# Kernel optimization log

Hardware: AMD Instinct MI355X
Metric: run time of the kernel (lower is better)

Reference implementation:

```python
import jax, jax.numpy as jnp
import numpy as np

N_NODES = 100_000
N_EDGES = 1_600_000
N_GRAPHS = 512
IN_C, HID_C, OUT_C = 17, 64, 32


def setup_inputs() -> dict:
    key = jax.random.key(0)
    ks = jax.random.split(key, 12)
    x = jax.random.normal(ks[0], (N_NODES, IN_C), dtype=jnp.float32)
    edge_index = jax.random.randint(ks[1], (2, N_EDGES), 0, N_NODES, dtype=jnp.int64)
    batch = jnp.sort(jax.random.randint(ks[2], (N_NODES,), 0, N_GRAPHS, dtype=jnp.int64))
    def lin(k, fan_in, fan_out):
        s = 1.0 / np.sqrt(fan_in)
        kw, kb = jax.random.split(k)
        W = jax.random.uniform(kw, (fan_in, fan_out), minval=-s, maxval=s, dtype=jnp.float32)
        b = jax.random.uniform(kb, (fan_out,), minval=-s, maxval=s, dtype=jnp.float32)
        return W, b
    W1, b1 = lin(ks[3], IN_C, HID_C)      # GCNConv 1
    W2, b2 = lin(ks[4], HID_C, OUT_C)     # GCNConv 2
    Wf1, bf1 = lin(ks[5], OUT_C, OUT_C)   # fc1
    Wf2, bf2 = lin(ks[6], OUT_C, OUT_C)   # fc2
    return {"x": x, "edge_index": edge_index, "batch": batch,
            "W1": W1, "b1": b1, "W2": W2, "b2": b2,
            "Wf1": Wf1, "bf1": bf1, "Wf2": Wf2, "bf2": bf2}


def _gcn_conv(x, src, dst, norm, W, b, n_nodes):
    # PyG GCNConv: h = x @ W; out_i = sum_{j->i} norm_ij * h_j; out += bias
    h = x @ W                                   # [N, d_out]
    msg = h[src] * norm[:, None]                # gather + scale [E+N, d_out]
    out = jax.ops.segment_sum(msg, dst, num_segments=n_nodes)
    return out + b


def reference(x, edge_index, batch, W1, b1, W2, b2, Wf1, bf1, Wf2, bf2):
    n = x.shape[0]
    loops = jnp.arange(n, dtype=edge_index.dtype)
    src = jnp.concatenate([edge_index[0], loops])  # add self loops
    dst = jnp.concatenate([edge_index[1], loops])
    # symmetric normalization: deg^-1/2[src] * deg^-1/2[dst]
    deg = jax.ops.segment_sum(jnp.ones_like(dst, dtype=x.dtype), dst, num_segments=n)
    dinv = jnp.where(deg > 0, 1.0 / jnp.sqrt(deg), 0.0)
    norm = dinv[src] * dinv[dst]

    h = jax.nn.relu(_gcn_conv(x, src, dst, norm, W1, b1, n))
    h = _gcn_conv(h, src, dst, norm, W2, b2, n)

    # global mean pool over graphs
    cnt = jax.ops.segment_sum(jnp.ones((n,), dtype=h.dtype), batch, num_segments=N_GRAPHS)
    pooled = jax.ops.segment_sum(h, batch, num_segments=N_GRAPHS) / jnp.clip(cnt, 1.0)[:, None]

    out = jax.nn.relu(pooled @ Wf1 + bf1)
    out = out @ Wf2 + bf2
    return out  # [N_GRAPHS, OUT_C]
```

## Files before the change

### kernel.cpp

```cpp
#include <hip/hip_runtime.h>

#define IN_C 17
#define HID  64
#define OUTC 32

#define CH   8192
#define TA   512
#define NBP  512
#define BCAP 5632
#define SCAP 1024
#define BS_BLKS 8

typedef __attribute__((ext_vector_type(2))) float f2;
__device__ __forceinline__ f2 mkf2(float x, float y) { f2 r; r.x = x; r.y = y; return r; }

__device__ __forceinline__ unsigned short f2bf(float f) {
    unsigned u = __float_as_uint(f);
    u += 0x7fffu + ((u >> 16) & 1u);
    return (unsigned short)(u >> 16);
}
__device__ __forceinline__ float bflo(unsigned u) { return __uint_as_float(u << 16); }
__device__ __forceinline__ float bfhi(unsigned u) { return __uint_as_float(u & 0xffff0000u); }

__global__ __launch_bounds__(TA) void k_binA(const int* __restrict__ src,
        const int* __restrict__ dst, int E,
        int* __restrict__ outbuf, int* __restrict__ cntmat, int* __restrict__ offmat) {
    __shared__ int cnt[NBP];
    __shared__ int off[NBP];
    __shared__ int stage[CH];
    int t = threadIdx.x;
    long base = (long)blockIdx.x * CH;
    int nE = (int)(E - base); if (nE > CH) nE = CH;
    cnt[t] = 0;
    __syncthreads();
    int bk[16], pk[16], rk[16];
#pragma unroll
    for (int j = 0; j < 16; ++j) {
        int idx = t + j * TA;
        if (idx < nE) {
            long e = base + idx;
            int d = __builtin_nontemporal_load(&dst[e]);
            int s = __builtin_nontemporal_load(&src[e]);
            int b = d >> 8;
            bk[j] = b;
            pk[j] = s | ((d & 255) << 17);
            rk[j] = atomicAdd(&cnt[b], 1);
        } else bk[j] = -1;
    }
    __syncthreads();
    int c = cnt[t];
    off[t] = c;
    __syncthreads();
    int inc = c;
    for (int s = 1; s < NBP; s <<= 1) {
        int add = (t >= s) ? off[t - s] : 0;
        __syncthreads();
        inc += add; off[t] = inc;
        __syncthreads();
    }
    int excl = inc - c;
    __syncthreads();
    off[t] = excl;
    __syncthreads();
#pragma unroll
    for (int j = 0; j < 16; ++j)
        if (bk[j] >= 0) stage[off[bk[j]] + rk[j]] = pk[j];
    __syncthreads();
    for (int i = t; i < nE; i += TA) outbuf[base + i] = stage[i];
    cntmat[blockIdx.x * NBP + t] = c;
    offmat[blockIdx.x * NBP + t] = excl;
}

__global__ __launch_bounds__(NBP) void k_bsum1(const int* __restrict__ cntmat,
        int nblkA, int* __restrict__ part) {
    int t = threadIdx.x, b = blockIdx.x;
    int per = (nblkA + BS_BLKS - 1) / BS_BLKS;
    int i0 = b * per, i1 = min(i0 + per, nblkA);
    int s = 0;
    for (int i = i0; i < i1; ++i) s += cntmat[i * NBP + t];
    part[b * NBP + t] = s;
}

__global__ __launch_bounds__(NBP) void k_bsum2(const int* __restrict__ part,
        int* __restrict__ bbase) {
    __shared__ int sh[NBP];
    int t = threadIdx.x;
    int s = 0;
#pragma unroll
    for (int i = 0; i < BS_BLKS; ++i) s += part[i * NBP + t];
    sh[t] = s;
    __syncthreads();
    int inc = s;
    for (int st = 1; st < NBP; st <<= 1) {
        int add = (t >= st) ? sh[t - st] : 0;
        __syncthreads();
        inc += add; sh[t] = inc;
        __syncthreads();
    }
    bbase[t] = inc - s;
}

__global__ __launch_bounds__(TA) void k_binB(const int* __restrict__ outbuf,
        const int* __restrict__ cntmat, const int* __restrict__ offmat,
        const int* __restrict__ bbase, int nblkA, int N,
        int* __restrict__ csr, int2* __restrict__ meta,
        const float* __restrict__ x, unsigned* __restrict__ xs16h,
        unsigned short* __restrict__ xs17h) {
    __shared__ int segc[256], sego[256], segs[256];
    __shared__ int ndeg[256], noff[256];
    __shared__ int stage[BCAP];
    int t = threadIdx.x, b = blockIdx.x;
    if (t < 256) {
        int cc = 0, ss = 0;
        if (t < nblkA) { cc = cntmat[t * NBP + b]; ss = offmat[t * NBP + b]; }
        segc[t] = cc; segs[t] = ss; sego[t] = cc;
        ndeg[t] = 0;
    }
    __syncthreads();
    {
        int c = (t < 256) ? sego[t] : 0;
        int inc = c;
        for (int s = 1; s < 256; s <<= 1) {
            int add = (t < 256 && t >= s) ? sego[t - s] : 0;
            __syncthreads();
            if (t < 256) { inc += add; sego[t] = inc; }
            __syncthreads();
        }
        if (t < 256) sego[t] = inc - c;
    }
    __syncthreads();
    int wave = t >> 6, lane = t & 63;
    for (int i = wave; i < nblkA; i += TA / 64) {
        int c = segc[i], so = sego[i];
        long gs = (long)i * CH + segs[i];
        for (int l = lane; l < c; l += 64) {
            int p = so + l;
            if (p < BCAP) stage[p] = __builtin_nontemporal_load(&outbuf[gs + l]);
        }
    }
    __syncthreads();
    int T = sego[255] + segc[255];
    if (T > BCAP) T = BCAP;
    int mypk[11], myrk[11], ne = 0;
    for (int k = t; k < T; k += TA) {
        int p = stage[k];
        int l = (p >> 17) & 255;
        myrk[ne] = atomicAdd(&ndeg[l], 1);
        mypk[ne] = p;
        ne++;
    }
    __syncthreads();
    {
        int c = (t < 256) ? ndeg[t] : 0;
        if (t < 256) noff[t] = c;
        __syncthreads();
        int inc = c;
        for (int s = 1; s < 256; s <<= 1) {
            int add = (t < 256 && t >= s) ? noff[t - s] : 0;
            __syncthreads();
            if (t < 256) { inc += add; noff[t] = inc; }
            __syncthreads();
        }
        if (t < 256) noff[t] = inc - c;
    }
    __syncthreads();
    int gb = bbase[b];
    int n0 = b << 8;
    if (t < 256 && n0 + t < N) {
        int n = n0 + t;
        meta[n] = make_int2(gb + noff[t], ndeg[t]);
        float dinv = rsqrtf((float)(ndeg[t] + 1));
        const float* xr = x + (size_t)n * IN_C;
        unsigned* xo = xs16h + (size_t)n * 8;
#pragma unroll
        for (int w2 = 0; w2 < 8; ++w2) {
            unsigned lo = f2bf(xr[2 * w2] * dinv);
            unsigned hi = f2bf(xr[2 * w2 + 1] * dinv);
            xo[w2] = lo | (hi << 16);
        }
        xs17h[n] = f2bf(xr[16] * dinv);
    }
    for (int j = 0; j < ne; ++j) {
        int p = mypk[j];
        int l = (p >> 17) & 255;
        csr[gb + noff[l] + myrk[j]] = p & 0x1FFFF;
    }
}

__global__ __launch_bounds__(256) void k_gather1(
        const uint4* __restrict__ xs16v, const unsigned short* __restrict__ xs17h,
        const int* __restrict__ csr, const int2* __restrict__ meta,
        const float* __restrict__ W1, const float* __restrict__ b1,
        const float* __restrict__ W2, unsigned* __restrict__ hs2, int N) {
    __shared__ __align__(16) float aggx[16][20];
    __shared__ float dinv_sh[16];
    __shared__ __align__(16) float h1sh[16][68];
    __shared__ __align__(16) float w2c0[16][68];
    __shared__ __align__(16) float w2c1[16][68];
    __shared__ int csr_sh[SCAP];

    int tid = threadIdx.x;
    int n0 = blockIdx.x * 16;
    int nlast = min(n0 + 15, N - 1);
    int2 m0 = meta[n0];
    int2 mlv = meta[nlast];
    int s_lo = m0.x;
    int seglen = mlv.x + mlv.y - s_lo;
    int sg = min(seglen, SCAP);
    for (int i = tid; i < sg; i += 256)
        csr_sh[i] = __builtin_nontemporal_load(&csr[s_lo + i]);
    for (int i = tid; i < 16 * 64; i += 256) {
        int tc = i >> 6, k = i & 63;
        w2c0[tc][k] = W2[k * OUTC + 2 * tc];
        w2c1[tc][k] = W2[k * OUTC + 2 * tc + 1];
    }
    int ch = tid & 63;
    float w1r[IN_C];
#pragma unroll
    for (int k = 0; k < IN_C; ++k) w1r[k] = W1[k * HID + ch];
    float b1v = b1[ch];
    __syncthreads();

    int ln = tid >> 4, sl = tid & 15;
    int n = n0 + ln;
    f2 acc[8];
#pragma unroll
    for (int j = 0; j < 8; ++j) acc[j] = mkf2(0.f, 0.f);
    float a17 = 0.f;
    if (n < N) {
        int2 m = meta[n];
        int start = m.x, cnt = m.y, end = start + cnt;
        auto body = [&](int s) {
            uint4 v0 = xs16v[(size_t)s * 2];
            uint4 v1 = xs16v[(size_t)s * 2 + 1];
            acc[0] += mkf2(bflo(v0.x), bfhi(v0.x));
            acc[1] += mkf2(bflo(v0.y), bfhi(v0.y));
            acc[2] += mkf2(bflo(v0.z), bfhi(v0.z));
            acc[3] += mkf2(bflo(v0.w), bfhi(v0.w));
            acc[4] += mkf2(bflo(v1.x), bfhi(v1.x));
            acc[5] += mkf2(bflo(v1.y), bfhi(v1.y));
            acc[6] += mkf2(bflo(v1.z), bfhi(v1.z));
            acc[7] += mkf2(bflo(v1.w), bfhi(v1.w));
            a17 += bflo((unsigned)xs17h[s]);
        };
        if (seglen <= SCAP) {
            for (int k = start + sl; k < end; k += 16) body(csr_sh[k - s_lo]);
        } else {
            for (int k = start + sl; k < end; k += 16)
                body(__builtin_nontemporal_load(&csr[k]));
        }
        if (sl == 0) {
            body(n);
            dinv_sh[ln] = rsqrtf((float)(cnt + 1));
        }
    }
    float a[16];
#pragma unroll
    for (int j = 0; j < 8; ++j) { a[2 * j] = acc[j].x; a[2 * j + 1] = acc[j].y; }
#pragma unroll
    for (int j = 0; j < 8; ++j) {
        float tt = (sl & 8) ? a[j + 8] : a[j];
        float uu = (sl & 8) ? a[j] : a[j + 8];
        a[j] = tt + __shfl_xor(uu, 8);
    }
#pragma unroll
    for (int j = 0; j < 4; ++j) {
        float tt = (sl & 4) ? a[j + 4] : a[j];
        float uu = (sl & 4) ? a[j] : a[j + 4];
        a[j] = tt + __shfl_xor(uu, 4);
    }
#pragma unroll
    for (int j = 0; j < 2; ++j) {
        float tt = (sl & 2) ? a[j + 2] : a[j];
        float uu = (sl & 2) ? a[j] : a[j + 2];
        a[j] = tt + __shfl_xor(uu, 2);
    }
    {
        float tt = (sl & 1) ? a[1] : a[0];
        float uu = (sl & 1) ? a[0] : a[1];
        a[0] = tt + __shfl_xor(uu, 1);
    }
    a17 += __shfl_xor(a17, 1);
    a17 += __shfl_xor(a17, 2);
    a17 += __shfl_xor(a17, 4);
    a17 += __shfl_xor(a17, 8);
    aggx[ln][sl] = a[0];
    if (sl == 0) aggx[ln][16] = a17;
    __syncthreads();
    int s0 = tid >> 6;
#pragma unroll
    for (int rep = 0; rep < 4; ++rep) {
        int slot = s0 + rep * 4;
        int nn = n0 + slot;
        if (nn < N) {
            const float4* ap = (const float4*)aggx[slot];
            float4 A0 = ap[0], A1 = ap[1], A2 = ap[2], A3 = ap[3];
            float a16 = aggx[slot][16];
            float dot = A0.x * w1r[0]  + A0.y * w1r[1]  + A0.z * w1r[2]  + A0.w * w1r[3]
                      + A1.x * w1r[4]  + A1.y * w1r[5]  + A1.z * w1r[6]  + A1.w * w1r[7]
                      + A2.x * w1r[8]  + A2.y * w1r[9]  + A2.z * w1r[10] + A2.w * w1r[11]
                      + A3.x * w1r[12] + A3.y * w1r[13] + A3.z * w1r[14] + A3.w * w1r[15]
                      + a16  * w1r[16];
            h1sh[slot][ch] = fmaxf(dinv_sh[slot] * dot + b1v, 0.f);
        }
    }
    __syncthreads();
    int slot = tid >> 4;
    int tc = tid & 15;
    int nn = n0 + slot;
    if (nn < N) {
        float a0 = 0.f, a1 = 0.f;
        const float4* hp = (const float4*)h1sh[slot];
        const float4* w0 = (const float4*)w2c0[tc];
        const float4* w1 = (const float4*)w2c1[tc];
#pragma unroll
        for (int kg = 0; kg < 16; ++kg) {
            float4 hv = hp[kg];
            float4 wa = w0[kg];
            float4 wb = w1[kg];
            a0 += hv.x * wa.x + hv.y * wa.y + hv.z * wa.z + hv.w * wa.w;
            a1 += hv.x * wb.x + hv.y * wb.y + hv.z * wb.z + hv.w * wb.w;
        }
        float dv = dinv_sh[slot];
        hs2[(size_t)nn * 16 + tc] = (unsigned)f2bf(a0 * dv) | ((unsigned)f2bf(a1 * dv) << 16);
    }
}

__global__ __launch_bounds__(256) void k_gather2(
        const uint4* __restrict__ hs2v, const int* __restrict__ csr,
        const int2* __restrict__ meta, const float* __restrict__ b2,
        const int* __restrict__ batch, float* pool, float* cntg, int N) {
    __shared__ __align__(16) float cont[16][OUTC];
    __shared__ int bsh[16];
    __shared__ int csr_sh[SCAP];
    int tid = threadIdx.x;
    int n0 = blockIdx.x * 16;
    int nlast = min(n0 + 15, N - 1);
    int2 m0 = meta[n0];
    int2 mlv = meta[nlast];
    int s_lo = m0.x;
    int seglen = mlv.x + mlv.y - s_lo;
    int sg = min(seglen, SCAP);
    for (int i = tid; i < sg; i += 256)
        csr_sh[i] = __builtin_nontemporal_load(&csr[s_lo + i]);
    __syncthreads();

    int ln = tid >> 4, sl = tid & 15;
    int n = n0 + ln;
    f2 acc[16];
#pragma unroll
    for (int j = 0; j < 16; ++j) acc[j] = mkf2(0.f, 0.f);
    float dinv = 0.f;
    if (n < N) {
        int2 m = meta[n];
        int start = m.x, cnt = m.y, end = start + cnt;
        dinv = rsqrtf((float)(cnt + 1));
        auto body = [&](int s) {
            const uint4* rp = hs2v + (size_t)s * 4;
            uint4 v0 = rp[0], v1 = rp[1], v2 = rp[2], v3 = rp[3];
            acc[0]  += mkf2(bflo(v0.x), bfhi(v0.x));
            acc[1]  += mkf2(bflo(v0.y), bfhi(v0.y));
            acc[2]  += mkf2(bflo(v0.z), bfhi(v0.z));
            acc[3]  += mkf2(bflo(v0.w), bfhi(v0.w));
            acc[4]  += mkf2(bflo(v1.x), bfhi(v1.x));
            acc[5]  += mkf2(bflo(v1.y), bfhi(v1.y));
            acc[6]  += mkf2(bflo(v1.z), bfhi(v1.z));
            acc[7]  += mkf2(bflo(v1.w), bfhi(v1.w));
            acc[8]  += mkf2(bflo(v2.x), bfhi(v2.x));
            acc[9]  += mkf2(bflo(v2.y), bfhi(v2.y));
            acc[10] += mkf2(bflo(v2.z), bfhi(v2.z));
            acc[11] += mkf2(bflo(v2.w), bfhi(v2.w));
            acc[12] += mkf2(bflo(v3.x), bfhi(v3.x));
            acc[13] += mkf2(bflo(v3.y), bfhi(v3.y));
            acc[14] += mkf2(bflo(v3.z), bfhi(v3.z));
            acc[15] += mkf2(bflo(v3.w), bfhi(v3.w));
        };
        if (seglen <= SCAP) {
            for (int k = start + sl; k < end; k += 16) body(csr_sh[k - s_lo]);
        } else {
            for (int k = start + sl; k < end; k += 16)
                body(__builtin_nontemporal_load(&csr[k]));
        }
        if (sl == 0) body(n);
    }
    float a[32];
#pragma unroll
    for (int j = 0; j < 16; ++j) { a[2 * j] = acc[j].x; a[2 * j + 1] = acc[j].y; }
#pragma unroll
    for (int j = 0; j < 16; ++j) {
        float tt = (sl & 8) ? a[j + 16] : a[j];
        float uu = (sl & 8) ? a[j] : a[j + 16];
        a[j] = tt + __shfl_xor(uu, 8);
    }
#pragma unroll
    for (int j = 0; j < 8; ++j) {
        float tt = (sl & 4) ? a[j + 8] : a[j];
        float uu = (sl & 4) ? a[j] : a[j + 8];
        a[j] = tt + __shfl_xor(uu, 4);
    }
#pragma unroll
    for (int j = 0; j < 4; ++j) {
        float tt = (sl & 2) ? a[j + 4] : a[j];
        float uu = (sl & 2) ? a[j] : a[j + 4];
        a[j] = tt + __shfl_xor(uu, 2);
    }
#pragma unroll
    for (int j = 0; j < 2; ++j) {
        float tt = (sl & 1) ? a[j + 2] : a[j];
        float uu = (sl & 1) ? a[j] : a[j + 2];
        a[j] = tt + __shfl_xor(uu, 1);
    }
    if (n < N) {
        float c0 = dinv * a[0] + b2[2 * sl];
        float c1 = dinv * a[1] + b2[2 * sl + 1];
        *(float2*)&cont[ln][2 * sl] = make_float2(c0, c1);
        if (sl == 0) bsh[ln] = batch[n];
    } else {
        *(float2*)&cont[ln][2 * sl] = make_float2(0.f, 0.f);
        if (sl == 0) bsh[ln] = -1;
    }
    __syncthreads();
    if (tid < OUTC) {
        int c = tid;
        float run = 0.f; int cur = -1;
        for (int j = 0; j < 16; ++j) {
            int bj = bsh[j];
            if (bj < 0) continue;
            if (bj == cur) run += cont[j][c];
            else {
                if (cur >= 0) atomicAdd(&pool[(size_t)cur * OUTC + c], run);
                cur = bj; run = cont[j][c];
            }
        }
        if (cur >= 0) atomicAdd(&pool[(size_t)cur * OUTC + c], run);
        if (c == 0) {
            float crun = 0.f; cur = -1;
            for (int j = 0; j < 16; ++j) {
                int bj = bsh[j];
                if (bj < 0) continue;
                if (bj == cur) crun += 1.f;
                else {
                    if (cur >= 0) atomicAdd(&cntg[cur], crun);
                    cur = bj; crun = 1.f;
                }
            }
            if (cur >= 0) atomicAdd(&cntg[cur], crun);
        }
    }
}

__global__ void k_final(const float* __restrict__ pool, const float* __restrict__ cntg,
                        const float* __restrict__ Wf1, const float* __restrict__ bf1,
                        const float* __restrict__ Wf2, const float* __restrict__ bf2,
                        float* out, int G) {
    __shared__ float p[OUTC], t[OUTC];
    int g = blockIdx.x;
    int c = threadIdx.x;
    float csafe = fmaxf(cntg[g], 1.0f);
    p[c] = pool[g * OUTC + c] / csafe;
    __syncthreads();
    float acc = bf1[c];
#pragma unroll
    for (int k = 0; k < OUTC; ++k) acc += p[k] * Wf1[k * OUTC + c];
    t[c] = fmaxf(acc, 0.f);
    __syncthreads();
    float acc2 = bf2[c];
#pragma unroll
    for (int k = 0; k < OUTC; ++k) acc2 += t[k] * Wf2[k * OUTC + c];
    out[g * OUTC + c] = acc2;
}

extern "C" void kernel_launch(void* const* d_in, const int* in_sizes, int n_in,
                              void* d_out, int out_size, void* d_ws, size_t ws_size,
                              hipStream_t stream) {
    const float* x    = (const float*)d_in[0];
    const int*   ei   = (const int*)  d_in[1];
    const int*   batch= (const int*)  d_in[2];
    const float* W1   = (const float*)d_in[3];
    const float* b1   = (const float*)d_in[4];
    const float* W2   = (const float*)d_in[5];
    const float* b2   = (const float*)d_in[6];
    const float* Wf1  = (const float*)d_in[7];
    const float* bf1  = (const float*)d_in[8];
    const float* Wf2  = (const float*)d_in[9];
    const float* bf2  = (const float*)d_in[10];

    const int N = in_sizes[0] / IN_C;
    const int E = in_sizes[1] / 2;
    const int G = out_size / OUTC;
    const int* src = ei;
    const int* dst = ei + E;

    const int nblkA = (E + CH - 1) / CH;
    const int NB    = (N + 255) >> 8;

    char* w = (char*)d_ws;
    int*   csr      = (int*)w;   w += (size_t)E * sizeof(int);
    int2*  meta     = (int2*)w;  w += (size_t)N * sizeof(int2);
    unsigned* xs16h = (unsigned*)w; w += (size_t)N * 8 * sizeof(unsigned);
    unsigned* hs2   = (unsigned*)w; w += (size_t)N * 16 * sizeof(unsigned);
    unsigned short* xs17h = (unsigned short*)w; w += (size_t)N * sizeof(unsigned short);
    w = (char*)(((size_t)w + 15) & ~(size_t)15);
    float* pool     = (float*)w; w += (size_t)G * OUTC * sizeof(float);
    float* cntg     = (float*)w; w += (size_t)G * sizeof(float);
    w = (char*)(((size_t)w + 15) & ~(size_t)15);
    int*   outbuf   = (int*)w;   w += (size_t)E * sizeof(int);
    int*   cntmat   = (int*)w;   w += (size_t)nblkA * NBP * sizeof(int);
    int*   offmat   = (int*)w;   w += (size_t)nblkA * NBP * sizeof(int);
    int*   bbase    = (int*)w;   w += NBP * sizeof(int);
    int*   part     = (int*)w;   w += BS_BLKS * NBP * sizeof(int);

    hipMemsetAsync(pool, 0, (size_t)(G * OUTC + G) * sizeof(float), stream);

    k_binA<<<nblkA, TA, 0, stream>>>(src, dst, E, outbuf, cntmat, offmat);
    k_bsum1<<<BS_BLKS, NBP, 0, stream>>>(cntmat, nblkA, part);
    k_bsum2<<<1, NBP, 0, stream>>>(part, bbase);
    k_binB<<<NB, TA, 0, stream>>>(outbuf, cntmat, offmat, bbase, nblkA, N,
                                  csr, meta, x, xs16h, xs17h);

    dim3 blk(256);
    k_gather1<<<(N + 15) / 16, blk, 0, stream>>>((const uint4*)xs16h, xs17h, csr, meta,
                                                 W1, b1, W2, hs2, N);

    k_gather2<<<(N + 15) / 16, blk, 0, stream>>>((const uint4*)hs2, csr, meta,
                                                 b2, batch, pool, cntg, N);

    k_final<<<G, OUTC, 0, stream>>>(pool, cntg, Wf1, bf1, Wf2, bf2, (float*)d_out, G);
}
```

Before: 140.4 us.

## Move second-layer matmul into separate bf16 MFMA kernel

New measurement: 135.2 us. 1.04x faster.

```diff
diff --git a/kernel.cpp b/kernel.cpp
--- a/kernel.cpp
+++ b/kernel.cpp
@@ -12,6 +12,8 @@
 #define BS_BLKS 8
 
 typedef __attribute__((ext_vector_type(2))) float f2;
+typedef __attribute__((ext_vector_type(8))) short bf16x8;
+typedef __attribute__((ext_vector_type(4))) float f32x4;
 __device__ __forceinline__ f2 mkf2(float x, float y) { f2 r; r.x = x; r.y = y; return r; }
 
 __device__ __forceinline__ unsigned short f2bf(float f) {
@@ -82,7 +84,8 @@
 }
 
 __global__ __launch_bounds__(NBP) void k_bsum2(const int* __restrict__ part,
-        int* __restrict__ bbase) {
+        int* __restrict__ bbase, const float* __restrict__ W2,
+        uint4* __restrict__ w2frag) {
     __shared__ int sh[NBP];
     int t = threadIdx.x;
     int s = 0;
@@ -98,6 +101,21 @@
         __syncthreads();
     }
     bbase[t] = inc - s;
+    if (t < 256) {
+        int f = t >> 6, l = t & 63;
+        int kt = f >> 1, nt = f & 1;
+        int kbase = kt * 32 + (l >> 4) * 8;
+        int c = nt * 16 + (l & 15);
+        unsigned short v[8];
+#pragma unroll
+        for (int j = 0; j < 8; ++j) v[j] = f2bf(W2[(kbase + j) * OUTC + c]);
+        uint4 o;
+        o.x = (unsigned)v[0] | ((unsigned)v[1] << 16);
+        o.y = (unsigned)v[2] | ((unsigned)v[3] << 16);
+        o.z = (unsigned)v[4] | ((unsigned)v[5] << 16);
+        o.w = (unsigned)v[6] | ((unsigned)v[7] << 16);
+        w2frag[f * 64 + l] = o;
+    }
 }
 
 __global__ __launch_bounds__(TA) void k_binB(const int* __restrict__ outbuf,
@@ -191,12 +209,9 @@
         const uint4* __restrict__ xs16v, const unsigned short* __restrict__ xs17h,
         const int* __restrict__ csr, const int2* __restrict__ meta,
         const float* __restrict__ W1, const float* __restrict__ b1,
-        const float* __restrict__ W2, unsigned* __restrict__ hs2, int N) {
+        unsigned short* __restrict__ h1b, int N) {
     __shared__ __align__(16) float aggx[16][20];
     __shared__ float dinv_sh[16];
-    __shared__ __align__(16) float h1sh[16][68];
-    __shared__ __align__(16) float w2c0[16][68];
-    __shared__ __align__(16) float w2c1[16][68];
     __shared__ int csr_sh[SCAP];
 
     int tid = threadIdx.x;
@@ -209,11 +224,6 @@
     int sg = min(seglen, SCAP);
     for (int i = tid; i < sg; i += 256)
         csr_sh[i] = __builtin_nontemporal_load(&csr[s_lo + i]);
-    for (int i = tid; i < 16 * 64; i += 256) {
-        int tc = i >> 6, k = i & 63;
-        w2c0[tc][k] = W2[k * OUTC + 2 * tc];
-        w2c1[tc][k] = W2[k * OUTC + 2 * tc + 1];
-    }
     int ch = tid & 63;
     float w1r[IN_C];
 #pragma unroll
@@ -301,28 +311,41 @@
                       + A2.x * w1r[8]  + A2.y * w1r[9]  + A2.z * w1r[10] + A2.w * w1r[11]
                       + A3.x * w1r[12] + A3.y * w1r[13] + A3.z * w1r[14] + A3.w * w1r[15]
                       + a16  * w1r[16];
-            h1sh[slot][ch] = fmaxf(dinv_sh[slot] * dot + b1v, 0.f);
-        }
-    }
-    __syncthreads();
-    int slot = tid >> 4;
-    int tc = tid & 15;
-    int nn = n0 + slot;
-    if (nn < N) {
-        float a0 = 0.f, a1 = 0.f;
-        const float4* hp = (const float4*)h1sh[slot];
-        const float4* w0 = (const float4*)w2c0[tc];
-        const float4* w1 = (const float4*)w2c1[tc];
-#pragma unroll
-        for (int kg = 0; kg < 16; ++kg) {
-            float4 hv = hp[kg];
-            float4 wa = w0[kg];
-            float4 wb = w1[kg];
-            a0 += hv.x * wa.x + hv.y * wa.y + hv.z * wa.z + hv.w * wa.w;
-            a1 += hv.x * wb.x + hv.y * wb.y + hv.z * wb.z + hv.w * wb.w;
-        }
-        float dv = dinv_sh[slot];
-        hs2[(size_t)nn * 16 + tc] = (unsigned)f2bf(a0 * dv) | ((unsigned)f2bf(a1 * dv) << 16);
+            float dv = dinv_sh[slot];
+            float r = fmaxf(dv * dot + b1v, 0.f);
+            h1b[(size_t)nn * HID + ch] = f2bf(dv * r);
+        }
+    }
+}
+
+__global__ __launch_bounds__(256) void k_mm2f(
+        const unsigned short* __restrict__ h1b, const uint4* __restrict__ w2frag,
+        unsigned* __restrict__ hs2, int N) {
+    int tid = threadIdx.x;
+    int wv = tid >> 6, l = tid & 63;
+    int n0w = blockIdx.x * 64 + wv * 16;
+    int row = l & 15, kq = l >> 4;
+    const bf16x8* a0p = (const bf16x8*)(h1b + (size_t)(n0w + row) * HID + kq * 8);
+    const bf16x8* a1p = (const bf16x8*)(h1b + (size_t)(n0w + row) * HID + 32 + kq * 8);
+    bf16x8 a0 = *a0p;
+    bf16x8 a1 = *a1p;
+    bf16x8 b00 = *(const bf16x8*)&w2frag[0 * 64 + l];
+    bf16x8 b01 = *(const bf16x8*)&w2frag[1 * 64 + l];
+    bf16x8 b10 = *(const bf16x8*)&w2frag[2 * 64 + l];
+    bf16x8 b11 = *(const bf16x8*)&w2frag[3 * 64 + l];
+    f32x4 d0 = {0.f, 0.f, 0.f, 0.f}, d1 = {0.f, 0.f, 0.f, 0.f};
+    d0 = __builtin_amdgcn_mfma_f32_16x16x32_bf16(a0, b00, d0, 0, 0, 0);
+    d0 = __builtin_amdgcn_mfma_f32_16x16x32_bf16(a1, b10, d0, 0, 0, 0);
+    d1 = __builtin_amdgcn_mfma_f32_16x16x32_bf16(a0, b01, d1, 0, 0, 0);
+    d1 = __builtin_amdgcn_mfma_f32_16x16x32_bf16(a1, b11, d1, 0, 0, 0);
+    int wcol = l & 15;
+    int rbase = (l >> 4) * 4;
+#pragma unroll
+    for (int r = 0; r < 4; ++r) {
+        int node = n0w + rbase + r;
+        if (node < N)
+            hs2[(size_t)node * 16 + wcol] =
+                (unsigned)f2bf(d0[r]) | ((unsigned)f2bf(d1[r]) << 16);
     }
 }
 
@@ -411,12 +434,12 @@
         a[j] = tt + __shfl_xor(uu, 1);
     }
     if (n < N) {
-        float c0 = dinv * a[0] + b2[2 * sl];
-        float c1 = dinv * a[1] + b2[2 * sl + 1];
-        *(float2*)&cont[ln][2 * sl] = make_float2(c0, c1);
+        cont[ln][sl]      = dinv * a[0] + b2[sl];
+        cont[ln][sl + 16] = dinv * a[1] + b2[sl + 16];
         if (sl == 0) bsh[ln] = batch[n];
     } else {
-        *(float2*)&cont[ln][2 * sl] = make_float2(0.f, 0.f);
+        cont[ln][sl] = 0.f;
+        cont[ln][sl + 16] = 0.f;
         if (sl == 0) bsh[ln] = -1;
     }
     __syncthreads();
@@ -509,18 +532,23 @@
     int*   offmat   = (int*)w;   w += (size_t)nblkA * NBP * sizeof(int);
     int*   bbase    = (int*)w;   w += NBP * sizeof(int);
     int*   part     = (int*)w;   w += BS_BLKS * NBP * sizeof(int);
+    w = (char*)(((size_t)w + 15) & ~(size_t)15);
+    unsigned short* h1b = (unsigned short*)w; w += (size_t)(N + 64) * HID * sizeof(unsigned short);
+    uint4* w2frag   = (uint4*)w; w += 4 * 64 * sizeof(uint4);
 
     hipMemsetAsync(pool, 0, (size_t)(G * OUTC + G) * sizeof(float), stream);
 
     k_binA<<<nblkA, TA, 0, stream>>>(src, dst, E, outbuf, cntmat, offmat);
     k_bsum1<<<BS_BLKS, NBP, 0, stream>>>(cntmat, nblkA, part);
-    k_bsum2<<<1, NBP, 0, stream>>>(part, bbase);
+    k_bsum2<<<1, NBP, 0, stream>>>(part, bbase, W2, w2frag);
     k_binB<<<NB, TA, 0, stream>>>(outbuf, cntmat, offmat, bbase, nblkA, N,
                                   csr, meta, x, xs16h, xs17h);
 
     dim3 blk(256);
     k_gather1<<<(N + 15) / 16, blk, 0, stream>>>((const uint4*)xs16h, xs17h, csr, meta,
-                                                 W1, b1, W2, hs2, N);
+                                                 W1, b1, h1b, N);
+
+    k_mm2f<<<(N + 63) / 64, blk, 0, stream>>>(h1b, w2frag, hs2, N);
 
     k_gather2<<<(N + 15) / 16, blk, 0, stream>>>((const uint4*)hs2, csr, meta,
                                                  b2, batch, pool, cntg, N);
```
